# Optimization experiments

Hardware: AMD Instinct MI355X
Metric: run time of the kernel (lower is better)

## Reference

```python
import jax, jax.numpy as jnp
import numpy as np

NUM_EXPERTS = 8
HIDDEN = 2048
EXPERT_DIM = 4096
TOK_PER_EXPERT = 1024


def setup_inputs() -> dict:
    key = jax.random.key(0)
    k1, k2, k3 = jax.random.split(key, 3)
    hidden_states = jax.random.normal(k1, (NUM_EXPERTS * TOK_PER_EXPERT, HIDDEN), dtype=jnp.float32)
    gate_up_proj = jax.random.normal(k2, (NUM_EXPERTS, HIDDEN, 2 * EXPERT_DIM), dtype=jnp.float32)
    down_proj = jax.random.normal(k3, (NUM_EXPERTS, EXPERT_DIM, HIDDEN), dtype=jnp.float32)
    return {"hidden_states": hidden_states, "gate_up_proj": gate_up_proj, "down_proj": down_proj}


def reference(hidden_states, gate_up_proj, down_proj):
    E, H = gate_up_proj.shape[0], gate_up_proj.shape[1]
    x = hidden_states.reshape(E, -1, H)            # [E, T, H]
    gate_up = jnp.einsum('eth,ehf->etf', x, gate_up_proj)  # [E, T, 2I]
    gate, up = jnp.split(gate_up, 2, axis=-1)
    gated = up * jax.nn.silu(gate)                 # [E, T, I]
    out = jnp.einsum('eti,eih->eth', gated, down_proj)     # [E, T, H]
    return out.reshape(-1, H)
```

## Files before the change

### kernel.cpp

```cpp
#include <hip/hip_runtime.h>

#define NE   8
#define TPE  1024
#define HID  2048
#define EXD  4096
#define FF   8192

typedef short short8 __attribute__((ext_vector_type(8)));
typedef float f32x4 __attribute__((ext_vector_type(4)));

__device__ __forceinline__ unsigned int pk2bf(float a, float b) {
  unsigned int ua = __float_as_uint(a);
  unsigned int ub = __float_as_uint(b);
  ua = (ua + 0x7fffu + ((ua >> 16) & 1u)) >> 16;
  ub = (ub + 0x7fffu + ((ub >> 16) & 1u)) >> 16;
  return ua | (ub << 16);
}

__device__ __forceinline__ unsigned short f2bf(float a) {
  unsigned int ua = __float_as_uint(a);
  return (unsigned short)((ua + 0x7fffu + ((ua >> 16) & 1u)) >> 16);
}

__global__ __launch_bounds__(256) void gemm1_silu(
    const float* __restrict__ x, const float* __restrict__ w1,
    unsigned short* __restrict__ gated) {
  __shared__ unsigned short As[128 * 32];
  __shared__ unsigned short Bg[128 * 32];
  __shared__ unsigned short Bu[128 * 32];

  const int e  = blockIdx.z;
  const int t0 = blockIdx.y * 128;
  const int i0 = blockIdx.x * 128;
  const int t  = threadIdx.x;
  const int lane = t & 63, wv = t >> 6, wm = wv & 1, wn = wv >> 1;

  const float* xA  = x  + (size_t)(e * TPE + t0) * HID;
  const float* w1e = w1 + (size_t)e * HID * FF;

  const int mA = t >> 1, hA = t & 1;
  const int nB = t & 127, gB = t >> 7;

  f32x4 accg[4][4], accu[4][4];
  const f32x4 vzero = {0.f, 0.f, 0.f, 0.f};
  #pragma unroll
  for (int a = 0; a < 4; ++a)
    #pragma unroll
    for (int b = 0; b < 4; ++b) { accg[a][b] = vzero; accu[a][b] = vzero; }

  for (int k0 = 0; k0 < HID; k0 += 32) {
    {
      const float* ap = xA + (size_t)mA * HID + k0 + hA * 16;
      float4 a0 = *(const float4*)(ap + 0);
      float4 a1 = *(const float4*)(ap + 4);
      float4 a2 = *(const float4*)(ap + 8);
      float4 a3 = *(const float4*)(ap + 12);
      uint4 p0, p1;
      p0.x = pk2bf(a0.x, a0.y); p0.y = pk2bf(a0.z, a0.w);
      p0.z = pk2bf(a1.x, a1.y); p0.w = pk2bf(a1.z, a1.w);
      p1.x = pk2bf(a2.x, a2.y); p1.y = pk2bf(a2.z, a2.w);
      p1.z = pk2bf(a3.x, a3.y); p1.w = pk2bf(a3.z, a3.w);
      *(uint4*)&As[mA * 32 + hA * 16 + 0] = p0;
      *(uint4*)&As[mA * 32 + hA * 16 + 8] = p1;
    }
    #pragma unroll
    for (int it = 0; it < 2; ++it) {
      const int kb = gB * 8 + it * 16;
      const float* bp = w1e + (size_t)(k0 + kb) * FF + i0 + nB;
      float gv[8], uv[8];
      #pragma unroll
      for (int r = 0; r < 8; ++r) {
        gv[r] = bp[(size_t)r * FF];
        uv[r] = bp[(size_t)r * FF + EXD];
      }
      uint4 pg, pu;
      pg.x = pk2bf(gv[0], gv[1]); pg.y = pk2bf(gv[2], gv[3]);
      pg.z = pk2bf(gv[4], gv[5]); pg.w = pk2bf(gv[6], gv[7]);
      pu.x = pk2bf(uv[0], uv[1]); pu.y = pk2bf(uv[2], uv[3]);
      pu.z = pk2bf(uv[4], uv[5]); pu.w = pk2bf(uv[6], uv[7]);
      *(uint4*)&Bg[nB * 32 + kb] = pg;
      *(uint4*)&Bu[nB * 32 + kb] = pu;
    }
    __syncthreads();

    short8 af[4], bgf[4], buf2[4];
    #pragma unroll
    for (int mi = 0; mi < 4; ++mi)
      af[mi] = *(const short8*)&As[(wm * 64 + mi * 16 + (lane & 15)) * 32 + (lane >> 4) * 8];
    #pragma unroll
    for (int ni = 0; ni < 4; ++ni) {
      const int ro = (wn * 64 + ni * 16 + (lane & 15)) * 32 + (lane >> 4) * 8;
      bgf[ni] = *(const short8*)&Bg[ro];
      buf2[ni] = *(const short8*)&Bu[ro];
    }
    #pragma unroll
    for (int mi = 0; mi < 4; ++mi)
      #pragma unroll
      for (int ni = 0; ni < 4; ++ni) {
        accg[mi][ni] = __builtin_amdgcn_mfma_f32_16x16x32_bf16(af[mi], bgf[ni], accg[mi][ni], 0, 0, 0);
        accu[mi][ni] = __builtin_amdgcn_mfma_f32_16x16x32_bf16(af[mi], buf2[ni], accu[mi][ni], 0, 0, 0);
      }
    __syncthreads();
  }

  const int r0 = t0 + wm * 64;
  const int c0 = i0 + wn * 64;
  const int qr = (lane >> 4) * 4, cl = lane & 15;
  #pragma unroll
  for (int mi = 0; mi < 4; ++mi)
    #pragma unroll
    for (int ni = 0; ni < 4; ++ni)
      #pragma unroll
      for (int v = 0; v < 4; ++v) {
        const int r = r0 + mi * 16 + qr + v;
        const int c = c0 + ni * 16 + cl;
        const float g = accg[mi][ni][v];
        const float u = accu[mi][ni][v];
        const float s = g / (1.f + __expf(-g));
        gated[(size_t)(e * TPE + r) * EXD + c] = f2bf(u * s);
      }
}

__global__ __launch_bounds__(256) void gemm2(
    const unsigned short* __restrict__ gated, const float* __restrict__ w2,
    float* __restrict__ out) {
  __shared__ unsigned short As[128 * 32];
  __shared__ unsigned short Bs[128 * 32];

  const int e  = blockIdx.z;
  const int t0 = blockIdx.y * 128;
  const int h0 = blockIdx.x * 128;
  const int t  = threadIdx.x;
  const int lane = t & 63, wv = t >> 6, wm = wv & 1, wn = wv >> 1;

  const unsigned short* Ae = gated + (size_t)(e * TPE + t0) * EXD;
  const float* w2e = w2 + (size_t)e * EXD * HID;

  const int arow = t >> 2, ac8 = (t & 3) * 8;
  const int nB = t & 127, gB = t >> 7;

  f32x4 acc[4][4];
  const f32x4 vzero = {0.f, 0.f, 0.f, 0.f};
  #pragma unroll
  for (int a = 0; a < 4; ++a)
    #pragma unroll
    for (int b = 0; b < 4; ++b) acc[a][b] = vzero;

  for (int k0 = 0; k0 < EXD; k0 += 32) {
    #pragma unroll
    for (int rr = 0; rr < 2; ++rr) {
      const unsigned short* gp = Ae + (size_t)(rr * 64 + arow) * EXD + k0 + ac8;
      *(uint4*)&As[rr * 2048 + t * 8] = *(const uint4*)gp;
    }
    #pragma unroll
    for (int it = 0; it < 2; ++it) {
      const int kb = gB * 8 + it * 16;
      const float* bp = w2e + (size_t)(k0 + kb) * HID + h0 + nB;
      float bv[8];
      #pragma unroll
      for (int r = 0; r < 8; ++r) bv[r] = bp[(size_t)r * HID];
      uint4 pb;
      pb.x = pk2bf(bv[0], bv[1]); pb.y = pk2bf(bv[2], bv[3]);
      pb.z = pk2bf(bv[4], bv[5]); pb.w = pk2bf(bv[6], bv[7]);
      *(uint4*)&Bs[nB * 32 + kb] = pb;
    }
    __syncthreads();

    short8 af[4], bfr[4];
    #pragma unroll
    for (int mi = 0; mi < 4; ++mi)
      af[mi] = *(const short8*)&As[(wm * 64 + mi * 16 + (lane & 15)) * 32 + (lane >> 4) * 8];
    #pragma unroll
    for (int ni = 0; ni < 4; ++ni)
      bfr[ni] = *(const short8*)&Bs[(wn * 64 + ni * 16 + (lane & 15)) * 32 + (lane >> 4) * 8];
    #pragma unroll
    for (int mi = 0; mi < 4; ++mi)
      #pragma unroll
      for (int ni = 0; ni < 4; ++ni)
        acc[mi][ni] = __builtin_amdgcn_mfma_f32_16x16x32_bf16(af[mi], bfr[ni], acc[mi][ni], 0, 0, 0);
    __syncthreads();
  }

  const int r0 = t0 + wm * 64;
  const int c0 = h0 + wn * 64;
  const int qr = (lane >> 4) * 4, cl = lane & 15;
  #pragma unroll
  for (int mi = 0; mi < 4; ++mi)
    #pragma unroll
    for (int ni = 0; ni < 4; ++ni)
      #pragma unroll
      for (int v = 0; v < 4; ++v) {
        const int r = r0 + mi * 16 + qr + v;
        const int c = c0 + ni * 16 + cl;
        out[(size_t)(e * TPE + r) * HID + c] = acc[mi][ni][v];
      }
}

extern "C" void kernel_launch(void* const* d_in, const int* in_sizes, int n_in,
                              void* d_out, int out_size, void* d_ws, size_t ws_size,
                              hipStream_t stream) {
  const float* x  = (const float*)d_in[0];
  const float* w1 = (const float*)d_in[1];
  const float* w2 = (const float*)d_in[2];
  float* out = (float*)d_out;
  unsigned short* gated = (unsigned short*)d_ws;

  dim3 blk(256, 1, 1);
  dim3 g1(EXD / 128, TPE / 128, NE);
  dim3 g2(HID / 128, TPE / 128, NE);
  gemm1_silu<<<g1, blk, 0, stream>>>(x, w1, gated);
  gemm2<<<g2, blk, 0, stream>>>(gated, w2, out);
}
```

Baseline: 2.002 ms.

## Pre-convert inputs to bf16 with transposed weights and use direct-to-LDS loads

Adds prepass kernels that convert activations to bf16 and transpose-convert both weight tensors to bf16 in K-contiguous layout inside the workspace. New GEMM kernels then stage tiles through global_load_lds 16-byte copies, with no per-tile fp32 loads and in-loop packing. This removes the strided column reads and the repeated conversion of each weight tile across every token block, at the cost of extra prepass traffic and a large workspace requirement. If the workspace is too small it falls back to the old kernels.

```diff
diff --git a/kernel.cpp b/kernel.cpp
--- a/kernel.cpp
+++ b/kernel.cpp
@@ -20,6 +20,196 @@
 __device__ __forceinline__ unsigned short f2bf(float a) {
   unsigned int ua = __float_as_uint(a);
   return (unsigned short)((ua + 0x7fffu + ((ua >> 16) & 1u)) >> 16);
+}
+
+__device__ __forceinline__ void gload_lds16(const unsigned short* g, unsigned short* l) {
+  typedef __attribute__((address_space(1))) unsigned int GU;
+  typedef __attribute__((address_space(3))) unsigned int LU;
+  __builtin_amdgcn_global_load_lds((const GU*)g, (LU*)l, 16, 0, 0);
+}
+
+__global__ __launch_bounds__(256) void convert_bf16(
+    const float* __restrict__ in, unsigned short* __restrict__ out, int n8) {
+  const int i = blockIdx.x * 256 + threadIdx.x;
+  if (i >= n8) return;
+  const float4 a0 = *(const float4*)(in + (size_t)i * 8);
+  const float4 a1 = *(const float4*)(in + (size_t)i * 8 + 4);
+  uint4 p;
+  p.x = pk2bf(a0.x, a0.y); p.y = pk2bf(a0.z, a0.w);
+  p.z = pk2bf(a1.x, a1.y); p.w = pk2bf(a1.z, a1.w);
+  *(uint4*)(out + (size_t)i * 8) = p;
+}
+
+__global__ __launch_bounds__(256) void transpose_cvt(
+    const float* __restrict__ in, unsigned short* __restrict__ out, int R, int C) {
+  __shared__ unsigned short lt[64 * 64];
+  const int e = blockIdx.z;
+  const int r0 = blockIdx.y * 64, c0 = blockIdx.x * 64;
+  const int t = threadIdx.x;
+  const float* ie = in + (size_t)e * R * C;
+  unsigned short* oe = out + (size_t)e * R * C;
+  const int ty = t >> 4, tx = t & 15;
+  #pragma unroll
+  for (int it = 0; it < 2; ++it) {
+    const int kr = it * 32 + ty * 2;
+    const float* p0 = ie + (size_t)(r0 + kr) * C + c0 + tx * 4;
+    const float4 a0 = *(const float4*)p0;
+    const float4 a1 = *(const float4*)(p0 + C);
+    *(unsigned int*)&lt[(tx * 4 + 0) * 64 + kr] = pk2bf(a0.x, a1.x);
+    *(unsigned int*)&lt[(tx * 4 + 1) * 64 + kr] = pk2bf(a0.y, a1.y);
+    *(unsigned int*)&lt[(tx * 4 + 2) * 64 + kr] = pk2bf(a0.z, a1.z);
+    *(unsigned int*)&lt[(tx * 4 + 3) * 64 + kr] = pk2bf(a0.w, a1.w);
+  }
+  __syncthreads();
+  const int f = t >> 3, ch = t & 7;
+  #pragma unroll
+  for (int p = 0; p < 2; ++p) {
+    const int fo = p * 32 + f;
+    const uint4 v = *(const uint4*)&lt[fo * 64 + ch * 8];
+    *(uint4*)(oe + (size_t)(c0 + fo) * R + r0 + ch * 8) = v;
+  }
+}
+
+__global__ __launch_bounds__(256) void gemm1_silu_bf(
+    const unsigned short* __restrict__ xbf,
+    const unsigned short* __restrict__ w1t,
+    unsigned short* __restrict__ gated) {
+  __shared__ unsigned short As[128 * 32];
+  __shared__ unsigned short Bg[128 * 32];
+  __shared__ unsigned short Bu[128 * 32];
+
+  const int e  = blockIdx.z;
+  const int t0 = blockIdx.y * 128;
+  const int i0 = blockIdx.x * 128;
+  const int t  = threadIdx.x;
+  const int lane = t & 63, wv = t >> 6, wm = wv & 1, wn = wv >> 1;
+
+  const unsigned short* xA  = xbf + (size_t)(e * TPE + t0) * HID;
+  const unsigned short* w1e = w1t + (size_t)e * FF * HID;
+
+  const int srow = lane >> 2;
+  const int scol = (lane & 3) * 8;
+
+  f32x4 accg[4][4], accu[4][4];
+  const f32x4 vzero = {0.f, 0.f, 0.f, 0.f};
+  #pragma unroll
+  for (int a = 0; a < 4; ++a)
+    #pragma unroll
+    for (int b = 0; b < 4; ++b) { accg[a][b] = vzero; accu[a][b] = vzero; }
+
+  for (int k0 = 0; k0 < HID; k0 += 32) {
+    #pragma unroll
+    for (int c = 0; c < 2; ++c) {
+      const int rb = wv * 32 + c * 16;
+      const int r  = rb + srow;
+      gload_lds16(xA  + (size_t)r * HID + k0 + scol,               &As[rb * 32]);
+      gload_lds16(w1e + (size_t)(i0 + r) * HID + k0 + scol,        &Bg[rb * 32]);
+      gload_lds16(w1e + (size_t)(EXD + i0 + r) * HID + k0 + scol,  &Bu[rb * 32]);
+    }
+    __syncthreads();
+
+    short8 af[4], bgf[4], buf2[4];
+    #pragma unroll
+    for (int mi = 0; mi < 4; ++mi)
+      af[mi] = *(const short8*)&As[(wm * 64 + mi * 16 + (lane & 15)) * 32 + (lane >> 4) * 8];
+    #pragma unroll
+    for (int ni = 0; ni < 4; ++ni) {
+      const int ro = (wn * 64 + ni * 16 + (lane & 15)) * 32 + (lane >> 4) * 8;
+      bgf[ni]  = *(const short8*)&Bg[ro];
+      buf2[ni] = *(const short8*)&Bu[ro];
+    }
+    #pragma unroll
+    for (int mi = 0; mi < 4; ++mi)
+      #pragma unroll
+      for (int ni = 0; ni < 4; ++ni) {
+        accg[mi][ni] = __builtin_amdgcn_mfma_f32_16x16x32_bf16(af[mi], bgf[ni], accg[mi][ni], 0, 0, 0);
+        accu[mi][ni] = __builtin_amdgcn_mfma_f32_16x16x32_bf16(af[mi], buf2[ni], accu[mi][ni], 0, 0, 0);
+      }
+    __syncthreads();
+  }
+
+  const int r0 = t0 + wm * 64;
+  const int c0 = i0 + wn * 64;
+  const int qr = (lane >> 4) * 4, cl = lane & 15;
+  #pragma unroll
+  for (int mi = 0; mi < 4; ++mi)
+    #pragma unroll
+    for (int ni = 0; ni < 4; ++ni)
+      #pragma unroll
+      for (int v = 0; v < 4; ++v) {
+        const int r = r0 + mi * 16 + qr + v;
+        const int c = c0 + ni * 16 + cl;
+        const float g = accg[mi][ni][v];
+        const float u = accu[mi][ni][v];
+        const float s = g / (1.f + __expf(-g));
+        gated[(size_t)(e * TPE + r) * EXD + c] = f2bf(u * s);
+      }
+}
+
+__global__ __launch_bounds__(256) void gemm2_bf(
+    const unsigned short* __restrict__ gated,
+    const unsigned short* __restrict__ w2t,
+    float* __restrict__ out) {
+  __shared__ unsigned short As[128 * 32];
+  __shared__ unsigned short Bs[128 * 32];
+
+  const int e  = blockIdx.z;
+  const int t0 = blockIdx.y * 128;
+  const int h0 = blockIdx.x * 128;
+  const int t  = threadIdx.x;
+  const int lane = t & 63, wv = t >> 6, wm = wv & 1, wn = wv >> 1;
+
+  const unsigned short* Ae  = gated + (size_t)(e * TPE + t0) * EXD;
+  const unsigned short* w2e = w2t + (size_t)e * HID * EXD;
+
+  const int srow = lane >> 2;
+  const int scol = (lane & 3) * 8;
+
+  f32x4 acc[4][4];
+  const f32x4 vzero = {0.f, 0.f, 0.f, 0.f};
+  #pragma unroll
+  for (int a = 0; a < 4; ++a)
+    #pragma unroll
+    for (int b = 0; b < 4; ++b) acc[a][b] = vzero;
+
+  for (int k0 = 0; k0 < EXD; k0 += 32) {
+    #pragma unroll
+    for (int c = 0; c < 2; ++c) {
+      const int rb = wv * 32 + c * 16;
+      const int r  = rb + srow;
+      gload_lds16(Ae  + (size_t)r * EXD + k0 + scol,        &As[rb * 32]);
+      gload_lds16(w2e + (size_t)(h0 + r) * EXD + k0 + scol, &Bs[rb * 32]);
+    }
+    __syncthreads();
+
+    short8 af[4], bfr[4];
+    #pragma unroll
+    for (int mi = 0; mi < 4; ++mi)
+      af[mi] = *(const short8*)&As[(wm * 64 + mi * 16 + (lane & 15)) * 32 + (lane >> 4) * 8];
+    #pragma unroll
+    for (int ni = 0; ni < 4; ++ni)
+      bfr[ni] = *(const short8*)&Bs[(wn * 64 + ni * 16 + (lane & 15)) * 32 + (lane >> 4) * 8];
+    #pragma unroll
+    for (int mi = 0; mi < 4; ++mi)
+      #pragma unroll
+      for (int ni = 0; ni < 4; ++ni)
+        acc[mi][ni] = __builtin_amdgcn_mfma_f32_16x16x32_bf16(af[mi], bfr[ni], acc[mi][ni], 0, 0, 0);
+    __syncthreads();
+  }
+
+  const int r0 = t0 + wm * 64;
+  const int c0 = h0 + wn * 64;
+  const int qr = (lane >> 4) * 4, cl = lane & 15;
+  #pragma unroll
+  for (int mi = 0; mi < 4; ++mi)
+    #pragma unroll
+    for (int ni = 0; ni < 4; ++ni)
+      #pragma unroll
+      for (int v = 0; v < 4; ++v) {
+        const int r = r0 + mi * 16 + qr + v;
+        const int c = c0 + ni * 16 + cl;
+        out[(size_t)(e * TPE + r) * HID + c] = acc[mi][ni][v];
+      }
 }
 
 __global__ __launch_bounds__(256) void gemm1_silu(
@@ -203,11 +393,30 @@
   const float* w1 = (const float*)d_in[1];
   const float* w2 = (const float*)d_in[2];
   float* out = (float*)d_out;
-  unsigned short* gated = (unsigned short*)d_ws;
+
+  const size_t SZ_XBF = (size_t)NE * TPE * HID * 2;
+  const size_t SZ_W1T = (size_t)NE * FF  * HID * 2;
+  const size_t SZ_W2T = (size_t)NE * HID * EXD * 2;
+  const size_t SZ_G   = (size_t)NE * TPE * EXD * 2;
+  const size_t REQ = SZ_XBF + SZ_W1T + SZ_W2T + SZ_G;
 
   dim3 blk(256, 1, 1);
-  dim3 g1(EXD / 128, TPE / 128, NE);
-  dim3 g2(HID / 128, TPE / 128, NE);
-  gemm1_silu<<<g1, blk, 0, stream>>>(x, w1, gated);
-  gemm2<<<g2, blk, 0, stream>>>(gated, w2, out);
-}
+
+  if (ws_size >= REQ) {
+    unsigned short* xbf   = (unsigned short*)d_ws;
+    unsigned short* w1t   = xbf + SZ_XBF / 2;
+    unsigned short* w2t   = w1t + SZ_W1T / 2;
+    unsigned short* gated = w2t + SZ_W2T / 2;
+
+    const int n8 = NE * TPE * HID / 8;
+    convert_bf16<<<dim3(n8 / 256, 1, 1), blk, 0, stream>>>(x, xbf, n8);
+    transpose_cvt<<<dim3(FF / 64, HID / 64, NE), blk, 0, stream>>>(w1, w1t, HID, FF);
+    transpose_cvt<<<dim3(HID / 64, EXD / 64, NE), blk, 0, stream>>>(w2, w2t, EXD, HID);
+    gemm1_silu_bf<<<dim3(EXD / 128, TPE / 128, NE), blk, 0, stream>>>(xbf, w1t, gated);
+    gemm2_bf<<<dim3(HID / 128, TPE / 128, NE), blk, 0, stream>>>(gated, w2t, out);
+  } else {
+    unsigned short* gated = (unsigned short*)d_ws;
+    gemm1_silu<<<dim3(EXD / 128, TPE / 128, NE), blk, 0, stream>>>(x, w1, gated);
+    gemm2<<<dim3(HID / 128, TPE / 128, NE), blk, 0, stream>>>(gated, w2, out);
+  }
+}
```

Measured after the change: 1.819 ms. 1.1x faster.
